# Optimization experiments

Hardware: AMD Instinct MI355X
Metric: run time of the kernel (lower is better)

Reference implementation:

```python
import jax, jax.numpy as jnp
import numpy as np

B, NE, NS, NI, NIS, H, NL = 8192, 210, 7, 8, 2, 128, 3


def setup_inputs() -> dict:
    key = jax.random.key(0)
    ks = jax.random.split(key, 24)
    inp = {}
    inp["F_dist"] = jax.random.normal(ks[0], (B, 45), jnp.float32)
    inp["F_cos"] = jax.random.normal(ks[1], (B, NE), jnp.float32)
    inp["F_sin"] = jax.random.normal(ks[2], (B, NE), jnp.float32)
    inp["F_angle"] = jax.random.normal(ks[3], (B, 8), jnp.float32)
    # Zscore tables: row 0 = mean, row 1 = std (kept away from zero)
    def zscore(k, f):
        k1, k2 = jax.random.split(k)
        mean = jax.random.normal(k1, (1, f), jnp.float32)
        std = jax.random.uniform(k2, (1, f), jnp.float32, 0.5, 1.5)
        return jnp.concatenate([mean, std], axis=0)
    inp["Zscore_dist"] = zscore(ks[4], 45)
    inp["Zscore_cos"] = zscore(ks[5], NE)
    inp["Zscore_sin"] = zscore(ks[6], NE)
    # per-expert index tables
    inp["INDEX3_4BD"] = jax.random.randint(ks[7], (NE, 6), 0, 45, jnp.int32)
    inp["INDEX5"] = jax.random.randint(ks[8], (NS,), 0, NE, jnp.int32)
    # 210 experts: Linear(8,H) + (NL-1)x Linear(H,H) + Linear(H,1), all tanh-separated
    s = 0.1
    inp["W1"] = jax.random.normal(ks[9], (NE, NI, H), jnp.float32) * s
    inp["b1"] = jax.random.normal(ks[10], (NE, H), jnp.float32) * s
    inp["Wh"] = jax.random.normal(ks[11], (NL - 1, NE, H, H), jnp.float32) * s
    inp["bh"] = jax.random.normal(ks[12], (NL - 1, NE, H), jnp.float32) * s
    inp["Wo"] = jax.random.normal(ks[13], (NE, H, 1), jnp.float32) * s
    inp["bo"] = jax.random.normal(ks[14], (NE, 1), jnp.float32) * s
    # 7 small experts: Linear(2,H) + (NL-1)x Linear(H,H) + Linear(H,1)
    inp["W1s"] = jax.random.normal(ks[15], (NS, NIS, H), jnp.float32) * s
    inp["b1s"] = jax.random.normal(ks[16], (NS, H), jnp.float32) * s
    inp["Whs"] = jax.random.normal(ks[17], (NL - 1, NS, H, H), jnp.float32) * s
    inp["bhs"] = jax.random.normal(ks[18], (NL - 1, NS, H), jnp.float32) * s
    inp["Wos"] = jax.random.normal(ks[19], (NS, H, 1), jnp.float32) * s
    inp["bos"] = jax.random.normal(ks[20], (NS, 1), jnp.float32) * s
    return inp


def _expert_stack(F, W1, b1, Wh, bh, Wo, bo):
    # F: [B, E, ni] -> [B, E, 1]; grouped tiny MLPs with tanh
    h = jnp.tanh(jnp.einsum("bei,eih->beh", F, W1) + b1)
    for l in range(Wh.shape[0]):
        h = jnp.tanh(jnp.einsum("beh,ehg->beg", h, Wh[l]) + bh[l])
    return jnp.einsum("beh,eho->beo", h, Wo) + bo


def reference(F_dist, F_cos, F_sin, F_angle, Zscore_dist, Zscore_cos, Zscore_sin,
              INDEX3_4BD, INDEX5,
              W1, b1, Wh, bh, Wo, bo, W1s, b1s, Whs, bhs, Wos, bos):
    FNorm_dist = (F_dist - Zscore_dist[0]) / Zscore_dist[1]  # [B,45]
    FNorm_cos = (F_cos - Zscore_cos[0]) / Zscore_cos[1]      # [B,210]
    FNorm_sin = (F_sin - Zscore_sin[0]) / Zscore_sin[1]      # [B,210]
    # gather per-expert 6 dist features + own cos/sin -> [B,210,8]
    Fd = FNorm_dist[:, INDEX3_4BD]                            # [B,210,6]
    F = jnp.concatenate([Fd, FNorm_cos[:, :, None], FNorm_sin[:, :, None]], axis=-1)
    out = _expert_stack(F, W1, b1, Wh, bh, Wo, bo)            # [B,210,1]
    total = jnp.sum(out, axis=1)                              # [B,1]
    # 7 small experts on (cos, sin) pairs picked by INDEX5
    Fs = jnp.stack([FNorm_cos[:, INDEX5], FNorm_sin[:, INDEX5]], axis=-1)  # [B,7,2]
    outs = _expert_stack(Fs, W1s, b1s, Whs, bhs, Wos, bos)    # [B,7,1]
    total = total + jnp.sum(outs, axis=1)
    return total
```

## Files before the change

### kernel.cpp

```cpp
#include <hip/hip_runtime.h>
#include <hip/hip_bf16.h>
#include <stdint.h>

#define NB 8192
#define NE 210
#define NS 7
#define NEXP 217
#define NI 8
#define H 128
#define BT 256
#define NTILE (NB / BT)
#define BLOB_STRIDE 71680
#define BIAS_OFF 4096
#define WH0_OFF 6144
#define WH1_OFF 38912
#define SMEM_BYTES 67584
#define K2 2.8853900817779268f

#define O_BLOB 0u
#define O_P2   15560000u
#define O_F    16000000u
#define O_FS   43525120u
#define O_PART 43754496u

typedef __attribute__((ext_vector_type(8))) short bf16x8;
typedef __attribute__((ext_vector_type(4))) float f32x4;
typedef __attribute__((ext_vector_type(16))) float f32x16;
typedef __attribute__((ext_vector_type(2))) int i32x2;

union I4V { int4 i; bf16x8 v; unsigned u[4]; };
union C16 { f32x16 v; f32x4 q[4]; };

__device__ __forceinline__ unsigned short f2bf(float f) {
  unsigned u = __float_as_uint(f);
  u += 0x7fffu + ((u >> 16) & 1u);
  return (unsigned short)(u >> 16);
}
__device__ __forceinline__ float fast_tanh_s(float xs) {
  float e = __builtin_amdgcn_exp2f(xs);
  return 1.0f - 2.0f * __builtin_amdgcn_rcpf(1.0f + e);
}
__device__ __forceinline__ unsigned pk_bf16(float a, float b) {
  unsigned r;
  asm("v_cvt_pk_bf16_f32 %0, %1, %2" : "=v"(r) : "v"(a), "v"(b));
  return r;
}
__device__ __forceinline__ void glds16(const void* g, void* l) {
  __builtin_amdgcn_global_load_lds(
      (const __attribute__((address_space(1))) unsigned int*)g,
      (__attribute__((address_space(3))) unsigned int*)l, 16, 0, 0);
}

__device__ __forceinline__ void transition(const f32x16 (&acc)[4], bf16x8 (&bn)[8]) {
#pragma unroll
  for (int kk = 0; kk < 8; ++kk) {
    const int ms = kk >> 1, ko = (kk & 1) * 8;
    unsigned P0 = pk_bf16(fast_tanh_s(acc[ms][ko + 0]), fast_tanh_s(acc[ms][ko + 1]));
    unsigned P1 = pk_bf16(fast_tanh_s(acc[ms][ko + 2]), fast_tanh_s(acc[ms][ko + 3]));
    unsigned P2 = pk_bf16(fast_tanh_s(acc[ms][ko + 4]), fast_tanh_s(acc[ms][ko + 5]));
    unsigned P3 = pk_bf16(fast_tanh_s(acc[ms][ko + 6]), fast_tanh_s(acc[ms][ko + 7]));
    i32x2 s0 = __builtin_amdgcn_permlane32_swap((int)P0, (int)P2, false, false);
    i32x2 s1 = __builtin_amdgcn_permlane32_swap((int)P1, (int)P3, false, false);
    I4V r;
    r.u[0] = (unsigned)s0.x;
    r.u[1] = (unsigned)s1.x;
    r.u[2] = (unsigned)s0.y;
    r.u[3] = (unsigned)s1.y;
    bn[kk] = r.v;
  }
}

__device__ __forceinline__ void hidden_layer(f32x16 (&acc)[4], const bf16x8 (&bn)[8],
                                             const uint8_t* wb, const float* biaL,
                                             int row, int hi, int hi4) {
  __builtin_amdgcn_s_setprio(1);
  {
    int soff0 = (hi ^ (row & 15)) << 4;
#pragma unroll
    for (int mt = 0; mt < 4; ++mt) {
      bf16x8 aF = *(const bf16x8*)(wb + (mt * 32 + row) * 256 + soff0);
      C16 c0;
#pragma unroll
      for (int i = 0; i < 4; ++i)
        c0.q[i] = *(const f32x4*)(biaL + mt * 32 + i * 8 + hi4);
      acc[mt] = __builtin_amdgcn_mfma_f32_32x32x16_bf16(aF, bn[0], c0.v, 0, 0, 0);
    }
  }
#pragma unroll
  for (int kk = 1; kk < 8; ++kk) {
    int soff = ((2 * kk + hi) ^ (row & 15)) << 4;
#pragma unroll
    for (int mt = 0; mt < 4; ++mt) {
      bf16x8 aF = *(const bf16x8*)(wb + (mt * 32 + row) * 256 + soff);
      acc[mt] = __builtin_amdgcn_mfma_f32_32x32x16_bf16(aF, bn[kk], acc[mt], 0, 0, 0);
    }
  }
  __builtin_amdgcn_s_setprio(0);
}

__global__ __launch_bounds__(256) void k_prep(
    const float* __restrict__ W1, const float* __restrict__ Wh,
    const float* __restrict__ W1s, const float* __restrict__ Whs,
    const float* __restrict__ bh, const float* __restrict__ bhs,
    const float* __restrict__ Wo, const float* __restrict__ Wos,
    const float* __restrict__ bo, const float* __restrict__ bos,
    const float* __restrict__ F_dist, const float* __restrict__ F_cos,
    const float* __restrict__ F_sin,
    const float* __restrict__ Zd, const float* __restrict__ Zc,
    const float* __restrict__ Zs,
    const int* __restrict__ IDX3, const int* __restrict__ IDX5,
    uint8_t* __restrict__ blob, uint16_t* __restrict__ F,
    uint16_t* __restrict__ Fs) {
  int bid = blockIdx.x;
  if (bid < NEXP * 3) {
    int n = threadIdx.x;
    if (n >= 128) return;
    int e = bid / 3, sec = bid % 3;
    uint8_t* be = blob + (size_t)e * BLOB_STRIDE;
    bool big = e < NE;
    int s = e - NE;
    if (sec == 0) {
      union { int4 v[2]; unsigned short u[16]; } row;
      row.v[0] = make_int4(0, 0, 0, 0);
      row.v[1] = make_int4(0, 0, 0, 0);
      if (big) {
        for (int k = 0; k < NI; ++k) row.u[k] = f2bf(K2 * W1[((size_t)e * NI + k) * H + n]);
      } else {
        for (int k = 0; k < 2; ++k) row.u[k] = f2bf(K2 * W1s[((size_t)s * 2 + k) * H + n]);
      }
      *(int4*)(be + n * 32) = row.v[0];
      *(int4*)(be + n * 32 + 16) = row.v[1];
      float* bsec = (float*)(be + BIAS_OFF);
      bsec[n]       = K2 * (big ? bh[(size_t)e * H + n]        : bhs[(size_t)s * H + n]);
      bsec[128 + n] = K2 * (big ? bh[((size_t)NE + e) * H + n] : bhs[((size_t)NS + s) * H + n]);
      bsec[256 + n] = big ? Wo[(size_t)e * H + n] : Wos[(size_t)s * H + n];
      if (n == 0) bsec[384] = big ? bo[e] : bos[s];
    } else {
      int l = sec - 1;
      union { int4 v[16]; unsigned short u[128]; } row;
      if (big) {
        for (int k = 0; k < H; ++k)
          row.u[k] = f2bf(K2 * Wh[(((size_t)l * NE + e) * H + k) * H + n]);
      } else {
        for (int k = 0; k < H; ++k)
          row.u[k] = f2bf(K2 * Whs[(((size_t)l * NS + s) * H + k) * H + n]);
      }
      int4* dst = (int4*)(be + (l ? WH1_OFF : WH0_OFF) + n * 256);
      for (int c = 0; c < 16; ++c) dst[c] = row.v[c ^ (n & 15)];
    }
  } else {
    int b2 = bid - NEXP * 3;
    int e = b2 >> 5, tile = b2 & 31;
    int b = tile * 256 + threadIdx.x;
    if (e < NE) {
      float cv = (F_cos[(size_t)b * NE + e] - Zc[e]) / Zc[NE + e];
      float sv = (F_sin[(size_t)b * NE + e] - Zs[e]) / Zs[NE + e];
      union { int4 v; unsigned short u[8]; } o;
      for (int j = 0; j < 6; ++j) {
        int id = IDX3[e * 6 + j];
        float x = (F_dist[(size_t)b * 45 + id] - Zd[id]) / Zd[45 + id];
        o.u[j] = f2bf(x);
      }
      o.u[6] = f2bf(cv);
      o.u[7] = f2bf(sv);
      *(int4*)(F + ((size_t)e * NB + b) * 8) = o.v;
    } else {
      int s = e - NE;
      int id = IDX5[s];
      float cv = (F_cos[(size_t)b * NE + id] - Zc[id]) / Zc[NE + id];
      float sv = (F_sin[(size_t)b * NE + id] - Zs[id]) / Zs[NE + id];
      unsigned o = (unsigned)f2bf(cv) | ((unsigned)f2bf(sv) << 16);
      *(unsigned*)(Fs + ((size_t)s * NB + b) * 2) = o;
    }
  }
}

__global__ __launch_bounds__(512, 4) void k_main(
    const uint8_t* __restrict__ blob,
    const uint16_t* __restrict__ F, const uint16_t* __restrict__ Fs,
    const float* __restrict__ b1, const float* __restrict__ b1s,
    float* __restrict__ partial) {
  extern __shared__ __attribute__((aligned(16))) uint8_t smem[];

  int bid = blockIdx.x;
  const int TOT = NEXP * NTILE;
  int lb = (bid & 7) * (TOT >> 3) + (bid >> 3);
  int e = lb >> 5;
  int tile = lb & 31;
  int brow = tile * BT;

  int t = threadIdx.x;
  int w = t >> 6, lane = t & 63;
  int row = lane & 31, hi = lane >> 5;
  int hi4 = hi << 2;

  bool big = e < NE;
  int s = e - NE;
  const uint8_t* be = blob + (size_t)e * BLOB_STRIDE;

  I4V bfr;
  bfr.i = make_int4(0, 0, 0, 0);
  if (hi == 0) {
    if (big) {
      bfr.i = *(const int4*)(F + ((size_t)e * NB + brow + w * 32 + row) * 8);
    } else {
      bfr.u[0] = *(const unsigned*)(Fs + ((size_t)s * NB + brow + w * 32 + row) * 2);
    }
  }
  const float* bias1 = big ? b1 + (size_t)e * H : b1s + (size_t)s * H;
  I4V aW[4];
  C16 c1[4];
#pragma unroll
  for (int mt = 0; mt < 4; ++mt) {
    aW[mt].i = *(const int4*)(be + (mt * 32 + row) * 32 + hi * 16);
#pragma unroll
    for (int i = 0; i < 4; ++i) {
      f32x4 q = *(const f32x4*)(bias1 + mt * 32 + i * 8 + hi4);
      c1[mt].q[i] = q * K2;
    }
  }
  __builtin_amdgcn_sched_barrier(0);

  for (int c = w; c < 34; c += 8)
    glds16(be + BIAS_OFF + c * 1024 + lane * 16, smem + c * 1024);
  __builtin_amdgcn_sched_barrier(0);
  for (int c = 34 + w; c < 66; c += 8)
    glds16(be + BIAS_OFF + c * 1024 + lane * 16, smem + c * 1024);
  __builtin_amdgcn_sched_barrier(0);

  f32x16 acc[4];
#pragma unroll
  for (int mt = 0; mt < 4; ++mt)
    acc[mt] = __builtin_amdgcn_mfma_f32_32x32x16_bf16(aW[mt].v, bfr.v, c1[mt].v, 0, 0, 0);

  bf16x8 bn[8];
  transition(acc, bn);

  asm volatile("s_waitcnt vmcnt(4)" ::: "memory");
  __builtin_amdgcn_s_barrier();
  __builtin_amdgcn_sched_barrier(0);

  hidden_layer(acc, bn, smem + 2048, (const float*)smem, row, hi, hi4);
  transition(acc, bn);

  asm volatile("s_waitcnt vmcnt(0)" ::: "memory");
  __builtin_amdgcn_s_barrier();
  __builtin_amdgcn_sched_barrier(0);

  hidden_layer(acc, bn, smem + 34816, (const float*)(smem + 512), row, hi, hi4);

  {
    const float* woL = (const float*)(smem + 1024);
    float bout = *(const float*)(smem + 1536);
    float sum = 0.f;
#pragma unroll
    for (int mt = 0; mt < 4; ++mt)
#pragma unroll
      for (int i = 0; i < 4; ++i) {
        f32x4 wq = *(const f32x4*)(woL + mt * 32 + i * 8 + hi4);
#pragma unroll
        for (int j = 0; j < 4; ++j)
          sum += fast_tanh_s(acc[mt][4 * i + j]) * wq[j];
      }
    sum += __shfl_xor(sum, 32);
    if (hi == 0)
      partial[(size_t)e * NB + brow + w * 32 + row] = sum + bout;
  }
}

__global__ __launch_bounds__(256) void k_reduce1(const float* __restrict__ partial,
                                                 float* __restrict__ partial2) {
  int g = blockIdx.x >> 5;
  int b = (blockIdx.x & 31) * 256 + threadIdx.x;
  const float* p = partial + (size_t)g * 31 * NB + b;
  float s = 0.f;
#pragma unroll
  for (int e = 0; e < 31; ++e) s += p[(size_t)e * NB];
  partial2[(size_t)g * NB + b] = s;
}
__global__ __launch_bounds__(256) void k_reduce2(const float* __restrict__ partial2,
                                                 float* __restrict__ out) {
  int b = blockIdx.x * 256 + threadIdx.x;
  float s = 0.f;
#pragma unroll
  for (int g = 0; g < 7; ++g) s += partial2[(size_t)g * NB + b];
  out[b] = s;
}

extern "C" void kernel_launch(void* const* d_in, const int* in_sizes, int n_in,
                              void* d_out, int out_size, void* d_ws, size_t ws_size,
                              hipStream_t stream) {
  const float* F_dist = (const float*)d_in[0];
  const float* F_cos  = (const float*)d_in[1];
  const float* F_sin  = (const float*)d_in[2];
  const float* Zd  = (const float*)d_in[4];
  const float* Zc  = (const float*)d_in[5];
  const float* Zs  = (const float*)d_in[6];
  const int* IDX3  = (const int*)d_in[7];
  const int* IDX5  = (const int*)d_in[8];
  const float* W1  = (const float*)d_in[9];
  const float* b1  = (const float*)d_in[10];
  const float* Wh  = (const float*)d_in[11];
  const float* bh  = (const float*)d_in[12];
  const float* Wo  = (const float*)d_in[13];
  const float* bo  = (const float*)d_in[14];
  const float* W1s = (const float*)d_in[15];
  const float* b1s = (const float*)d_in[16];
  const float* Whs = (const float*)d_in[17];
  const float* bhs = (const float*)d_in[18];
  const float* Wos = (const float*)d_in[19];
  const float* bos = (const float*)d_in[20];

  uint8_t* ws = (uint8_t*)d_ws;
  uint8_t* blob = ws + O_BLOB;
  float* partial2 = (float*)(ws + O_P2);
  uint16_t* F   = (uint16_t*)(ws + O_F);
  uint16_t* Fs  = (uint16_t*)(ws + O_FS);
  float* partial = (float*)(ws + O_PART);

  hipFuncSetAttribute(reinterpret_cast<const void*>(k_main),
                      hipFuncAttributeMaxDynamicSharedMemorySize, SMEM_BYTES);

  k_prep<<<NEXP * 3 + NEXP * 32, 256, 0, stream>>>(
      W1, Wh, W1s, Whs, bh, bhs, Wo, Wos, bo, bos,
      F_dist, F_cos, F_sin, Zd, Zc, Zs, IDX3, IDX5, blob, F, Fs);
  k_main<<<NEXP * NTILE, 512, SMEM_BYTES, stream>>>(blob, F, Fs, b1, b1s, partial);
  k_reduce1<<<7 * 32, 256, 0, stream>>>(partial, partial2);
  k_reduce2<<<NB / 256, 256, 0, stream>>>(partial2, (float*)d_out);
}
```

Baseline: 245.8 us.

## Fuse feature gather and z-score normalization into main expert kernel

Removes the per-expert feature materialization from the prep kernel, which wrote a bf16 [217,B,8] buffer (about 28 MB) and then had the main kernel read it back. The main kernel now gathers F_dist, F_cos and F_sin directly and normalizes them with precomputed scale and offset tables built by one extra prep block. This avoids the round trip through global memory and shrinks the prep grid, at the cost of uncoalesced strided gathers (stride 45 and 210 floats per row) inside the main kernel's prologue. It relies on a pk_bf16 helper that must exist in the unseen part of the file.

```diff
diff --git a/kernel.cpp b/kernel.cpp
--- a/kernel.cpp
+++ b/kernel.cpp
@@ -17,11 +17,16 @@
 #define SMEM_BYTES 67584
 #define K2 2.8853900817779268f
 
-#define O_BLOB 0u
+#define O_NORM 15556000u
 #define O_P2   15560000u
-#define O_F    16000000u
-#define O_FS   43525120u
 #define O_PART 43754496u
+
+#define N_AD 0
+#define N_BD 45
+#define N_AC 90
+#define N_BC 300
+#define N_AS 510
+#define N_BS 720
 
 typedef __attribute__((ext_vector_type(8))) short bf16x8;
 typedef __attribute__((ext_vector_type(4))) float f32x4;
@@ -104,80 +109,69 @@
     const float* __restrict__ bh, const float* __restrict__ bhs,
     const float* __restrict__ Wo, const float* __restrict__ Wos,
     const float* __restrict__ bo, const float* __restrict__ bos,
+    const float* __restrict__ Zd, const float* __restrict__ Zc,
+    const float* __restrict__ Zs,
+    uint8_t* __restrict__ blob, float* __restrict__ nrm) {
+  int bid = blockIdx.x;
+  if (bid == NEXP * 3) {
+    int t = threadIdx.x;
+    if (t < 45) {
+      float a = 1.0f / Zd[45 + t];
+      nrm[N_AD + t] = a;
+      nrm[N_BD + t] = -Zd[t] * a;
+    }
+    if (t < 210) {
+      float ac = 1.0f / Zc[NE + t];
+      nrm[N_AC + t] = ac;
+      nrm[N_BC + t] = -Zc[t] * ac;
+      float as = 1.0f / Zs[NE + t];
+      nrm[N_AS + t] = as;
+      nrm[N_BS + t] = -Zs[t] * as;
+    }
+    return;
+  }
+  int n = threadIdx.x;
+  if (n >= 128) return;
+  int e = bid / 3, sec = bid % 3;
+  uint8_t* be = blob + (size_t)e * BLOB_STRIDE;
+  bool big = e < NE;
+  int s = e - NE;
+  if (sec == 0) {
+    union { int4 v[2]; unsigned short u[16]; } row;
+    row.v[0] = make_int4(0, 0, 0, 0);
+    row.v[1] = make_int4(0, 0, 0, 0);
+    if (big) {
+      for (int k = 0; k < NI; ++k) row.u[k] = f2bf(K2 * W1[((size_t)e * NI + k) * H + n]);
+    } else {
+      for (int k = 0; k < 2; ++k) row.u[k] = f2bf(K2 * W1s[((size_t)s * 2 + k) * H + n]);
+    }
+    *(int4*)(be + n * 32) = row.v[0];
+    *(int4*)(be + n * 32 + 16) = row.v[1];
+    float* bsec = (float*)(be + BIAS_OFF);
+    bsec[n]       = K2 * (big ? bh[(size_t)e * H + n]        : bhs[(size_t)s * H + n]);
+    bsec[128 + n] = K2 * (big ? bh[((size_t)NE + e) * H + n] : bhs[((size_t)NS + s) * H + n]);
+    bsec[256 + n] = big ? Wo[(size_t)e * H + n] : Wos[(size_t)s * H + n];
+    if (n == 0) bsec[384] = big ? bo[e] : bos[s];
+  } else {
+    int l = sec - 1;
+    union { int4 v[16]; unsigned short u[128]; } row;
+    if (big) {
+      for (int k = 0; k < H; ++k)
+        row.u[k] = f2bf(K2 * Wh[(((size_t)l * NE + e) * H + k) * H + n]);
+    } else {
+      for (int k = 0; k < H; ++k)
+        row.u[k] = f2bf(K2 * Whs[(((size_t)l * NS + s) * H + k) * H + n]);
+    }
+    int4* dst = (int4*)(be + (l ? WH1_OFF : WH0_OFF) + n * 256);
+    for (int c = 0; c < 16; ++c) dst[c] = row.v[c ^ (n & 15)];
+  }
+}
+
+__global__ __launch_bounds__(512, 4) void k_main(
+    const uint8_t* __restrict__ blob, const float* __restrict__ nrm,
     const float* __restrict__ F_dist, const float* __restrict__ F_cos,
     const float* __restrict__ F_sin,
-    const float* __restrict__ Zd, const float* __restrict__ Zc,
-    const float* __restrict__ Zs,
     const int* __restrict__ IDX3, const int* __restrict__ IDX5,
-    uint8_t* __restrict__ blob, uint16_t* __restrict__ F,
-    uint16_t* __restrict__ Fs) {
-  int bid = blockIdx.x;
-  if (bid < NEXP * 3) {
-    int n = threadIdx.x;
-    if (n >= 128) return;
-    int e = bid / 3, sec = bid % 3;
-    uint8_t* be = blob + (size_t)e * BLOB_STRIDE;
-    bool big = e < NE;
-    int s = e - NE;
-    if (sec == 0) {
-      union { int4 v[2]; unsigned short u[16]; } row;
-      row.v[0] = make_int4(0, 0, 0, 0);
-      row.v[1] = make_int4(0, 0, 0, 0);
-      if (big) {
-        for (int k = 0; k < NI; ++k) row.u[k] = f2bf(K2 * W1[((size_t)e * NI + k) * H + n]);
-      } else {
-        for (int k = 0; k < 2; ++k) row.u[k] = f2bf(K2 * W1s[((size_t)s * 2 + k) * H + n]);
-      }
-      *(int4*)(be + n * 32) = row.v[0];
-      *(int4*)(be + n * 32 + 16) = row.v[1];
-      float* bsec = (float*)(be + BIAS_OFF);
-      bsec[n]       = K2 * (big ? bh[(size_t)e * H + n]        : bhs[(size_t)s * H + n]);
-      bsec[128 + n] = K2 * (big ? bh[((size_t)NE + e) * H + n] : bhs[((size_t)NS + s) * H + n]);
-      bsec[256 + n] = big ? Wo[(size_t)e * H + n] : Wos[(size_t)s * H + n];
-      if (n == 0) bsec[384] = big ? bo[e] : bos[s];
-    } else {
-      int l = sec - 1;
-      union { int4 v[16]; unsigned short u[128]; } row;
-      if (big) {
-        for (int k = 0; k < H; ++k)
-          row.u[k] = f2bf(K2 * Wh[(((size_t)l * NE + e) * H + k) * H + n]);
-      } else {
-        for (int k = 0; k < H; ++k)
-          row.u[k] = f2bf(K2 * Whs[(((size_t)l * NS + s) * H + k) * H + n]);
-      }
-      int4* dst = (int4*)(be + (l ? WH1_OFF : WH0_OFF) + n * 256);
-      for (int c = 0; c < 16; ++c) dst[c] = row.v[c ^ (n & 15)];
-    }
-  } else {
-    int b2 = bid - NEXP * 3;
-    int e = b2 >> 5, tile = b2 & 31;
-    int b = tile * 256 + threadIdx.x;
-    if (e < NE) {
-      float cv = (F_cos[(size_t)b * NE + e] - Zc[e]) / Zc[NE + e];
-      float sv = (F_sin[(size_t)b * NE + e] - Zs[e]) / Zs[NE + e];
-      union { int4 v; unsigned short u[8]; } o;
-      for (int j = 0; j < 6; ++j) {
-        int id = IDX3[e * 6 + j];
-        float x = (F_dist[(size_t)b * 45 + id] - Zd[id]) / Zd[45 + id];
-        o.u[j] = f2bf(x);
-      }
-      o.u[6] = f2bf(cv);
-      o.u[7] = f2bf(sv);
-      *(int4*)(F + ((size_t)e * NB + b) * 8) = o.v;
-    } else {
-      int s = e - NE;
-      int id = IDX5[s];
-      float cv = (F_cos[(size_t)b * NE + id] - Zc[id]) / Zc[NE + id];
-      float sv = (F_sin[(size_t)b * NE + id] - Zs[id]) / Zs[NE + id];
-      unsigned o = (unsigned)f2bf(cv) | ((unsigned)f2bf(sv) << 16);
-      *(unsigned*)(Fs + ((size_t)s * NB + b) * 2) = o;
-    }
-  }
-}
-
-__global__ __launch_bounds__(512, 4) void k_main(
-    const uint8_t* __restrict__ blob,
-    const uint16_t* __restrict__ F, const uint16_t* __restrict__ Fs,
     const float* __restrict__ b1, const float* __restrict__ b1s,
     float* __restrict__ partial) {
   extern __shared__ __attribute__((aligned(16))) uint8_t smem[];
@@ -201,10 +195,26 @@
   I4V bfr;
   bfr.i = make_int4(0, 0, 0, 0);
   if (hi == 0) {
+    int bb = brow + w * 32 + row;
     if (big) {
-      bfr.i = *(const int4*)(F + ((size_t)e * NB + brow + w * 32 + row) * 8);
+      const int* ix = IDX3 + e * 6;
+      float g[6];
+#pragma unroll
+      for (int j = 0; j < 6; ++j) {
+        int id = ix[j];
+        g[j] = __builtin_fmaf(F_dist[(size_t)bb * 45 + id], nrm[N_AD + id], nrm[N_BD + id]);
+      }
+      float cv = __builtin_fmaf(F_cos[(size_t)bb * NE + e], nrm[N_AC + e], nrm[N_BC + e]);
+      float sv = __builtin_fmaf(F_sin[(size_t)bb * NE + e], nrm[N_AS + e], nrm[N_BS + e]);
+      bfr.u[0] = pk_bf16(g[0], g[1]);
+      bfr.u[1] = pk_bf16(g[2], g[3]);
+      bfr.u[2] = pk_bf16(g[4], g[5]);
+      bfr.u[3] = pk_bf16(cv, sv);
     } else {
-      bfr.u[0] = *(const unsigned*)(Fs + ((size_t)s * NB + brow + w * 32 + row) * 2);
+      int id5 = IDX5[s];
+      float cv = __builtin_fmaf(F_cos[(size_t)bb * NE + id5], nrm[N_AC + id5], nrm[N_BC + id5]);
+      float sv = __builtin_fmaf(F_sin[(size_t)bb * NE + id5], nrm[N_AS + id5], nrm[N_BS + id5]);
+      bfr.u[0] = pk_bf16(cv, sv);
     }
   }
   const float* bias1 = big ? b1 + (size_t)e * H : b1s + (size_t)s * H;
@@ -312,19 +322,18 @@
   const float* bos = (const float*)d_in[20];
 
   uint8_t* ws = (uint8_t*)d_ws;
-  uint8_t* blob = ws + O_BLOB;
+  uint8_t* blob = ws;
+  float* nrm      = (float*)(ws + O_NORM);
   float* partial2 = (float*)(ws + O_P2);
-  uint16_t* F   = (uint16_t*)(ws + O_F);
-  uint16_t* Fs  = (uint16_t*)(ws + O_FS);
-  float* partial = (float*)(ws + O_PART);
+  float* partial  = (float*)(ws + O_PART);
 
   hipFuncSetAttribute(reinterpret_cast<const void*>(k_main),
                       hipFuncAttributeMaxDynamicSharedMemorySize, SMEM_BYTES);
 
-  k_prep<<<NEXP * 3 + NEXP * 32, 256, 0, stream>>>(
-      W1, Wh, W1s, Whs, bh, bhs, Wo, Wos, bo, bos,
-      F_dist, F_cos, F_sin, Zd, Zc, Zs, IDX3, IDX5, blob, F, Fs);
-  k_main<<<NEXP * NTILE, 512, SMEM_BYTES, stream>>>(blob, F, Fs, b1, b1s, partial);
+  k_prep<<<NEXP * 3 + 1, 256, 0, stream>>>(
+      W1, Wh, W1s, Whs, bh, bhs, Wo, Wos, bo, bos, Zd, Zc, Zs, blob, nrm);
+  k_main<<<NEXP * NTILE, 512, SMEM_BYTES, stream>>>(
+      blob, nrm, F_dist, F_cos, F_sin, IDX3, IDX5, b1, b1s, partial);
   k_reduce1<<<7 * 32, 256, 0, stream>>>(partial, partial2);
   k_reduce2<<<NB / 256, 256, 0, stream>>>(partial2, (float*)d_out);
 }
```

New measurement: 228.8 us. 6.9% less time.

## Gather normalized features in main kernel and reduce via atomics

Applied to the files above, without the earlier changes.

The prep kernel now writes normalized, transposed bf16 tables of dist, cos and sin features instead of a materialized per-expert gathered feature array. The main kernel gathers its 8 inputs through IDX3/IDX5 from these tables. The two reduction kernels are replaced by float atomicAdd into a zeroed output. This cuts the large per-expert feature write and read plus two launches, at the cost of scattered 2-byte loads in the main kernel, atomic contention on each output row, and a non-deterministic summation order.

```diff
diff --git a/kernel.cpp b/kernel.cpp
--- a/kernel.cpp
+++ b/kernel.cpp
@@ -17,11 +17,9 @@
 #define SMEM_BYTES 67584
 #define K2 2.8853900817779268f
 
-#define O_BLOB 0u
-#define O_P2   15560000u
-#define O_F    16000000u
-#define O_FS   43525120u
-#define O_PART 43754496u
+#define O_FT 15560000u
+#define O_CT 16300000u
+#define O_ST 19750000u
 
 typedef __attribute__((ext_vector_type(8))) short bf16x8;
 typedef __attribute__((ext_vector_type(4))) float f32x4;
@@ -108,9 +106,8 @@
     const float* __restrict__ F_sin,
     const float* __restrict__ Zd, const float* __restrict__ Zc,
     const float* __restrict__ Zs,
-    const int* __restrict__ IDX3, const int* __restrict__ IDX5,
-    uint8_t* __restrict__ blob, uint16_t* __restrict__ F,
-    uint16_t* __restrict__ Fs) {
+    uint8_t* __restrict__ blob, uint16_t* __restrict__ FT,
+    uint16_t* __restrict__ CT, uint16_t* __restrict__ ST) {
   int bid = blockIdx.x;
   if (bid < NEXP * 3) {
     int n = threadIdx.x;
@@ -148,38 +145,33 @@
       int4* dst = (int4*)(be + (l ? WH1_OFF : WH0_OFF) + n * 256);
       for (int c = 0; c < 16; ++c) dst[c] = row.v[c ^ (n & 15)];
     }
+  } else if (bid < NEXP * 3 + 32) {
+    int tile = bid - NEXP * 3;
+    int bb = tile * 256 + threadIdx.x;
+    for (int c = 0; c < 45; ++c) {
+      float a = 1.0f / Zd[45 + c];
+      FT[(size_t)c * NB + bb] = f2bf((F_dist[(size_t)bb * 45 + c] - Zd[c]) * a);
+    }
   } else {
-    int b2 = bid - NEXP * 3;
-    int e = b2 >> 5, tile = b2 & 31;
-    int b = tile * 256 + threadIdx.x;
-    if (e < NE) {
-      float cv = (F_cos[(size_t)b * NE + e] - Zc[e]) / Zc[NE + e];
-      float sv = (F_sin[(size_t)b * NE + e] - Zs[e]) / Zs[NE + e];
-      union { int4 v; unsigned short u[8]; } o;
-      for (int j = 0; j < 6; ++j) {
-        int id = IDX3[e * 6 + j];
-        float x = (F_dist[(size_t)b * 45 + id] - Zd[id]) / Zd[45 + id];
-        o.u[j] = f2bf(x);
-      }
-      o.u[6] = f2bf(cv);
-      o.u[7] = f2bf(sv);
-      *(int4*)(F + ((size_t)e * NB + b) * 8) = o.v;
-    } else {
-      int s = e - NE;
-      int id = IDX5[s];
-      float cv = (F_cos[(size_t)b * NE + id] - Zc[id]) / Zc[NE + id];
-      float sv = (F_sin[(size_t)b * NE + id] - Zs[id]) / Zs[NE + id];
-      unsigned o = (unsigned)f2bf(cv) | ((unsigned)f2bf(sv) << 16);
-      *(unsigned*)(Fs + ((size_t)s * NB + b) * 2) = o;
+    int idx = bid - NEXP * 3 - 32;
+    int chunk = idx >> 5, tile = idx & 31;
+    int bb = tile * 256 + threadIdx.x;
+    for (int c = chunk * 42; c < chunk * 42 + 42; ++c) {
+      float ac = 1.0f / Zc[NE + c];
+      CT[(size_t)c * NB + bb] = f2bf((F_cos[(size_t)bb * NE + c] - Zc[c]) * ac);
+      float as = 1.0f / Zs[NE + c];
+      ST[(size_t)c * NB + bb] = f2bf((F_sin[(size_t)bb * NE + c] - Zs[c]) * as);
     }
   }
 }
 
 __global__ __launch_bounds__(512, 4) void k_main(
     const uint8_t* __restrict__ blob,
-    const uint16_t* __restrict__ F, const uint16_t* __restrict__ Fs,
+    const uint16_t* __restrict__ FT, const uint16_t* __restrict__ CT,
+    const uint16_t* __restrict__ ST,
+    const int* __restrict__ IDX3, const int* __restrict__ IDX5,
     const float* __restrict__ b1, const float* __restrict__ b1s,
-    float* __restrict__ partial) {
+    float* __restrict__ out) {
   extern __shared__ __attribute__((aligned(16))) uint8_t smem[];
 
   int bid = blockIdx.x;
@@ -201,10 +193,26 @@
   I4V bfr;
   bfr.i = make_int4(0, 0, 0, 0);
   if (hi == 0) {
+    int bb = brow + w * 32 + row;
     if (big) {
-      bfr.i = *(const int4*)(F + ((size_t)e * NB + brow + w * 32 + row) * 8);
+      const int* ix = IDX3 + e * 6;
+      unsigned g0 = FT[(size_t)ix[0] * NB + bb];
+      unsigned g1 = FT[(size_t)ix[1] * NB + bb];
+      unsigned g2 = FT[(size_t)ix[2] * NB + bb];
+      unsigned g3 = FT[(size_t)ix[3] * NB + bb];
+      unsigned g4 = FT[(size_t)ix[4] * NB + bb];
+      unsigned g5 = FT[(size_t)ix[5] * NB + bb];
+      unsigned cv = CT[(size_t)e * NB + bb];
+      unsigned sv = ST[(size_t)e * NB + bb];
+      bfr.u[0] = g0 | (g1 << 16);
+      bfr.u[1] = g2 | (g3 << 16);
+      bfr.u[2] = g4 | (g5 << 16);
+      bfr.u[3] = cv | (sv << 16);
     } else {
-      bfr.u[0] = *(const unsigned*)(Fs + ((size_t)s * NB + brow + w * 32 + row) * 2);
+      int id5 = IDX5[s];
+      unsigned cv = CT[(size_t)id5 * NB + bb];
+      unsigned sv = ST[(size_t)id5 * NB + bb];
+      bfr.u[0] = cv | (sv << 16);
     }
   }
   const float* bias1 = big ? b1 + (size_t)e * H : b1s + (size_t)s * H;
@@ -264,27 +272,8 @@
       }
     sum += __shfl_xor(sum, 32);
     if (hi == 0)
-      partial[(size_t)e * NB + brow + w * 32 + row] = sum + bout;
-  }
-}
-
-__global__ __launch_bounds__(256) void k_reduce1(const float* __restrict__ partial,
-                                                 float* __restrict__ partial2) {
-  int g = blockIdx.x >> 5;
-  int b = (blockIdx.x & 31) * 256 + threadIdx.x;
-  const float* p = partial + (size_t)g * 31 * NB + b;
-  float s = 0.f;
-#pragma unroll
-  for (int e = 0; e < 31; ++e) s += p[(size_t)e * NB];
-  partial2[(size_t)g * NB + b] = s;
-}
-__global__ __launch_bounds__(256) void k_reduce2(const float* __restrict__ partial2,
-                                                 float* __restrict__ out) {
-  int b = blockIdx.x * 256 + threadIdx.x;
-  float s = 0.f;
-#pragma unroll
-  for (int g = 0; g < 7; ++g) s += partial2[(size_t)g * NB + b];
-  out[b] = s;
+      atomicAdd(out + brow + w * 32 + row, sum + bout);
+  }
 }
 
 extern "C" void kernel_launch(void* const* d_in, const int* in_sizes, int n_in,
@@ -312,19 +301,18 @@
   const float* bos = (const float*)d_in[20];
 
   uint8_t* ws = (uint8_t*)d_ws;
-  uint8_t* blob = ws + O_BLOB;
-  float* partial2 = (float*)(ws + O_P2);
-  uint16_t* F   = (uint16_t*)(ws + O_F);
-  uint16_t* Fs  = (uint16_t*)(ws + O_FS);
-  float* partial = (float*)(ws + O_PART);
+  uint8_t* blob = ws;
+  uint16_t* FT = (uint16_t*)(ws + O_FT);
+  uint16_t* CT = (uint16_t*)(ws + O_CT);
+  uint16_t* ST = (uint16_t*)(ws + O_ST);
 
   hipFuncSetAttribute(reinterpret_cast<const void*>(k_main),
                       hipFuncAttributeMaxDynamicSharedMemorySize, SMEM_BYTES);
 
-  k_prep<<<NEXP * 3 + NEXP * 32, 256, 0, stream>>>(
+  hipMemsetAsync(d_out, 0, (size_t)out_size * sizeof(float), stream);
+  k_prep<<<NEXP * 3 + 32 + 160, 256, 0, stream>>>(
       W1, Wh, W1s, Whs, bh, bhs, Wo, Wos, bo, bos,
-      F_dist, F_cos, F_sin, Zd, Zc, Zs, IDX3, IDX5, blob, F, Fs);
-  k_main<<<NEXP * NTILE, 512, SMEM_BYTES, stream>>>(blob, F, Fs, b1, b1s, partial);
-  k_reduce1<<<7 * 32, 256, 0, stream>>>(partial, partial2);
-  k_reduce2<<<NB / 256, 256, 0, stream>>>(partial2, (float*)d_out);
-}
+      F_dist, F_cos, F_sin, Zd, Zc, Zs, blob, FT, CT, ST);
+  k_main<<<NEXP * NTILE, 512, SMEM_BYTES, stream>>>(
+      blob, FT, CT, ST, IDX3, IDX5, b1, b1s, (float*)d_out);
+}
```

Measured after the change: 229.8 us. 6.5% less time.
